# Kernel optimization log

Hardware: AMD Instinct MI355X
Metric: run time of the kernel (lower is better)

The kernel has to match this reference:

```python
import jax, jax.numpy as jnp
import numpy as np

G, N, E = 16, 512, 2048        # graphs, nodes/graph, edges/graph
CN, CE = 64, 64                # node / edge feature channels
K = 3                          # Laguerre polynomial order
RATIO = 0.5
KEEP = int(np.ceil(RATIO * N)) # 256 kept nodes per graph (static)
POWER_ITERS = 64               # power iteration approximating eigsh(k=1,'LM')


def setup_inputs() -> dict:
    key = jax.random.key(0)
    ks = jax.random.split(key, 10)
    x_n = jax.random.normal(ks[0], (G * N, CN), jnp.float32)
    x_e = jax.random.normal(ks[1], (G * E, CE), jnp.float32)
    # incidence endpoints per edge, local node ids, no self loops
    u = jax.random.randint(ks[2], (G, E), 0, N)
    v = (u + 1 + jax.random.randint(ks[3], (G, E), 0, N - 1)) % N
    # node-level conv graph (global ids within per-graph blocks): both directions
    offs = (jnp.arange(G) * N)[:, None]
    src_n = jnp.concatenate([(u + offs).reshape(-1), (v + offs).reshape(-1)])
    dst_n = jnp.concatenate([(v + offs).reshape(-1), (u + offs).reshape(-1)])
    edge_weight_n = jax.random.uniform(ks[4], (src_n.shape[0],), jnp.float32)
    # edge-level conv graph (global ids within per-graph edge blocks)
    ME = 4 * E
    offs_e = (jnp.arange(G) * E)[:, None]
    src_e = (jax.random.randint(ks[5], (G, ME), 0, E) + offs_e).reshape(-1)
    dst_e = (jax.random.randint(ks[6], (G, ME), 0, E) + offs_e).reshape(-1)
    edge_weight_e = jax.random.uniform(ks[7], (src_e.shape[0],), jnp.float32)
    # HodgeLaguerreConv(C -> 1, K) weights (glorot-ish) + bias (zeros init)
    W_n = jax.random.normal(ks[8], (K, CN), jnp.float32) / np.sqrt(CN)
    b_n = jnp.zeros((1,), jnp.float32)
    W_e = jax.random.normal(ks[9], (K, CE), jnp.float32) / np.sqrt(CE)
    b_e = jnp.zeros((1,), jnp.float32)
    return dict(x_n=x_n, x_e=x_e, edge_u=u, edge_v=v,
                src_n=src_n, dst_n=dst_n, edge_weight_n=edge_weight_n,
                src_e=src_e, dst_e=dst_e, edge_weight_e=edge_weight_e,
                W_n=W_n, b_n=b_n, W_e=W_e, b_e=b_e)


def hodge_laguerre(x, src, dst, w, Wk, b):
    """HodgeLaguerreConv with out_channels=1: out = sum_k T_k(L) x @ Wk[k] + b.
    T_0 = x; T_1 = x - Lx; T_{k+1} = (-L T_k + (2k+1) T_k - k T_{k-1})/(k+1)."""
    num = x.shape[0]
    def L(z):  # scatter-add message passing: out[i] = sum_{j->i} norm * z[j]
        return jax.ops.segment_sum(w[:, None] * z[src], dst, num_segments=num)
    Tx0 = x
    out = Tx0 @ Wk[0]
    Tx1 = x - L(x)
    out = out + Tx1 @ Wk[1]
    k = 1
    for i in range(2, Wk.shape[0]):
        Tx2 = (-L(Tx1) + (2 * k + 1) * Tx1 - k * Tx0) / (k + 1)
        out = out + Tx2 @ Wk[i]
        Tx0, Tx1 = Tx1, Tx2
        k += 1
    return out + b[0]


def pool_graph(sn, se, xn, xe, u, v):
    # node score augmented by |B1| @ edge_score (abs incidence gathers both endpoints)
    aug = sn.at[u].add(se).at[v].add(se)
    perm = jnp.argsort(-aug)                    # descending sort, take top KEEP
    mask_n = jnp.zeros((N,), xn.dtype).at[perm[:KEEP]].set(1.0)
    # mask_e = |B1|^T (1 - mask_n); keep edge iff both endpoints kept (== 0)
    bad = (1.0 - mask_n[u]) + (1.0 - mask_n[v])
    keep_e = (bad == 0.0).astype(xn.dtype)
    # dense incidence B1 [N, E]: -1 at source row, +1 at target row
    cols = jnp.arange(E)
    B = jnp.zeros((N, E), xn.dtype).at[u, cols].add(-1.0).at[v, cols].add(1.0)
    Bm = B * mask_n[:, None] * keep_e[None, :]  # row/col masking (zero-padded)
    L0 = Bm @ Bm.T                              # [N, N] node Laplacian
    L1 = Bm.T @ Bm                              # [E, E] edge Laplacian
    # power iteration for lambda_max(L0) (== eigsh k=1 'LM'; zero rows keep spectrum)
    w = jnp.ones((N,), xn.dtype) / np.sqrt(N)
    for _ in range(POWER_ITERS):
        w = L0 @ w
        w = w / (jnp.linalg.norm(w) + 1e-12)
    lam = w @ (L0 @ w)
    scale = 2.0 / (lam + 1e-12)
    return xn * mask_n[:, None], L0 * scale, xe * keep_e[:, None], L1 * scale


def reference(x_n, x_e, edge_u, edge_v, src_n, dst_n, edge_weight_n,
              src_e, dst_e, edge_weight_e, W_n, b_n, W_e, b_e):
    score_n = jax.nn.sigmoid(hodge_laguerre(x_n, src_n, dst_n, edge_weight_n, W_n, b_n).reshape(-1))
    score_e = jax.nn.sigmoid(hodge_laguerre(x_e, src_e, dst_e, edge_weight_e, W_e, b_e).reshape(-1))
    xn_g = (x_n * score_n[:, None]).reshape(G, N, CN)
    xe_g = (x_e * score_e[:, None]).reshape(G, E, CE)
    sn = score_n.reshape(G, N)
    se = score_e.reshape(G, E)
    return jax.vmap(pool_graph)(sn, se, xn_g, xe_g, edge_u, edge_v)
```

## Files before the change

### kernel.cpp

```cpp
#include <hip/hip_runtime.h>
#include <math.h>

#define GG 16
#define NNODE 512
#define EEDGE 2048
#define KEEPN 256
#define PITERS 64
#define NNT 8192
#define NET 32768

#define WS_C1N 0
#define WS_C2N 8192
#define WS_BN  16384
#define WS_C1E 24576
#define WS_C2E 57344
#define WS_BE  90112
#define WS_SNW 122880
#define WS_SEW 131072
#define WS_KLIST 163840
#define WS_KCNT 196608
#define WS_SCALE 196624

#define O_XN 0
#define O_L0 524288
#define O_XE 4718592
#define O_L1 6815744

#define L04 1048576
#define ZTOT4 17825792

__global__ __launch_bounds__(256) void k_dots(const float* __restrict__ xn,
    const float* __restrict__ xe, const float* __restrict__ Wn,
    const float* __restrict__ We, float* __restrict__ ws) {
  int gw = (blockIdx.x * 256 + threadIdx.x) >> 6;
  int lane = threadIdx.x & 63;
  const float* x; const float* W; int row; float *c1, *c2, *bs;
  if (gw < NNT) {
    row = gw; x = xn + (size_t)row * 64; W = Wn;
    c1 = ws + WS_C1N; c2 = ws + WS_C2N; bs = ws + WS_BN;
  } else {
    row = gw - NNT;
    x = xe + (size_t)row * 64; W = We;
    c1 = ws + WS_C1E; c2 = ws + WS_C2E; bs = ws + WS_BE;
  }
  float v = x[lane];
  float r0 = v * W[lane];
  float r1 = v * W[64 + lane];
  float r2 = v * W[128 + lane];
  for (int o = 32; o; o >>= 1) {
    r0 += __shfl_xor(r0, o, 64);
    r1 += __shfl_xor(r1, o, 64);
    r2 += __shfl_xor(r2, o, 64);
  }
  if (lane == 0) { c1[row] = r1; c2[row] = r2; bs[row] = r0 + r1 + r2; }
}

#define SB 3104
__global__ __launch_bounds__(512) void k_pool(
    const int* __restrict__ src_n, const int* __restrict__ dst_n, const float* __restrict__ wn,
    const int* __restrict__ src_e, const int* __restrict__ dst_e, const float* __restrict__ we,
    const int* __restrict__ edge_u, const int* __restrict__ edge_v,
    const float* __restrict__ bnp, const float* __restrict__ bep,
    float* __restrict__ ws, float* __restrict__ out) {
  const int tid = threadIdx.x;
  if (blockIdx.x >= 16) {
    float4 z = make_float4(0.f, 0.f, 0.f, 0.f);
    float4* o4 = (float4*)out;
    int start = (blockIdx.x - 16) * 512 + tid;
    for (int i = start; i < ZTOT4; i += 2048 * 512) {
      int f = (i < L04) ? (O_L0 / 4 + i) : (O_L1 / 4 + (i - L04));
      o4[f] = z;
    }
    return;
  }
  __shared__ float smem[13856];
  int* smi = (int*)smem;
  float* seS = smem;
  float* aug = smem + 2048;
  float* snw = smem + 2560;
  float* red = smem + 3072;
  int*   iws = smi + 3080;
  int*   kcp = smi + 3088;
  float* c1n = smem + SB;        float* c2n = smem + SB + 512;
  float* d1n = smem + SB + 1024; float* d2n = smem + SB + 1536;
  float* e2n = smem + SB + 2048;
  float* c1e = smem + SB;        float* c2e = smem + SB + 2048;
  float* d1e = smem + SB + 4096; float* d2e = smem + SB + 6144;
  float* e2e = smem + SB + 8192;
  int* suL  = smi + SB;          int* svL  = smi + SB + 2048;
  int* maskS = smi + SB + 4096;  int* degS = smi + SB + 4608;
  int* offS = smi + SB + 5120;   int* adj  = smi + SB + 5632;
  float* wvA = smem + SB + 9728; float* wvB = smem + SB + 10240;

  const int g = blockIdx.x;
  const int roffN = g * NNODE;
  const int roffE = g * EEDGE;
  const int lane = tid & 63, wid = tid >> 6;

  if (tid < NNODE) {
    c1n[tid] = ws[WS_C1N + roffN + tid];
    c2n[tid] = ws[WS_C2N + roffN + tid];
    d1n[tid] = 0.f; d2n[tid] = 0.f; e2n[tid] = 0.f;
  }
  __syncthreads();
  for (int t = tid; t < 4096; t += 512) {
    int idx = (t < 2048) ? (g * 2048 + t) : (32768 + g * 2048 + (t - 2048));
    int s = src_n[idx] - roffN, d = dst_n[idx] - roffN;
    float w = wn[idx];
    atomicAdd(&d1n[d], w * c1n[s]);
    atomicAdd(&d2n[d], w * c2n[s]);
  }
  __syncthreads();
  for (int t = tid; t < 4096; t += 512) {
    int idx = (t < 2048) ? (g * 2048 + t) : (32768 + g * 2048 + (t - 2048));
    int s = src_n[idx] - roffN, d = dst_n[idx] - roffN;
    atomicAdd(&e2n[d], wn[idx] * d2n[s]);
  }
  __syncthreads();
  float biasN = bnp[0], biasE = bep[0];
  if (tid < NNODE) {
    float t = ws[WS_BN + roffN + tid] - d1n[tid] - 2.0f * d2n[tid]
            + 0.5f * e2n[tid] + biasN;
    float s = 1.0f / (1.0f + expf(-t));
    snw[tid] = s; aug[tid] = s;
  }
  __syncthreads();

  for (int i = tid; i < EEDGE; i += 512) {
    c1e[i] = ws[WS_C1E + roffE + i];
    c2e[i] = ws[WS_C2E + roffE + i];
    d1e[i] = 0.f; d2e[i] = 0.f; e2e[i] = 0.f;
  }
  __syncthreads();
  for (int t = tid; t < 8192; t += 512) {
    int idx = g * 8192 + t;
    int s = src_e[idx] - roffE, d = dst_e[idx] - roffE;
    float w = we[idx];
    atomicAdd(&d1e[d], w * c1e[s]);
    atomicAdd(&d2e[d], w * c2e[s]);
  }
  __syncthreads();
  for (int t = tid; t < 8192; t += 512) {
    int idx = g * 8192 + t;
    int s = src_e[idx] - roffE, d = dst_e[idx] - roffE;
    atomicAdd(&e2e[d], we[idx] * d2e[s]);
  }
  __syncthreads();
  for (int e = tid; e < EEDGE; e += 512) {
    float t = ws[WS_BE + roffE + e] - d1e[e] - 2.0f * d2e[e]
            + 0.5f * e2e[e] + biasE;
    float s = 1.0f / (1.0f + expf(-t));
    seS[e] = s;
    atomicAdd(&aug[edge_u[roffE + e]], s);
    atomicAdd(&aug[edge_v[roffE + e]], s);
  }
  __syncthreads();

  {
    float a = aug[tid];
    int r = 0;
    #pragma unroll 8
    for (int j = 0; j < NNODE; ++j) {
      float b = aug[j];
      r += (b > a) || (b == a && j < tid);
    }
    maskS[tid] = (r < KEEPN) ? 1 : 0;
    degS[tid] = 0;
  }
  for (int e = tid; e < EEDGE; e += 512) {
    suL[e] = edge_u[roffE + e];
    svL[e] = edge_v[roffE + e];
  }
  if (tid == 0) *kcp = 0;
  __syncthreads();
  ws[WS_SNW + roffN + tid] = snw[tid] * (float)maskS[tid];

  int* wsi = (int*)ws;
  for (int e = tid; e < EEDGE; e += 512) {
    int u = suL[e], v = svL[e];
    int k = maskS[u] & maskS[v];
    ws[WS_SEW + roffE + e] = seS[e] * (float)k;
    if (k) {
      int p = atomicAdd(kcp, 1);
      wsi[WS_KLIST + roffE + p] = e;
      atomicAdd(&degS[u], 1);
      atomicAdd(&degS[v], 1);
    }
  }
  __syncthreads();
  if (tid == 0) wsi[WS_KCNT + g] = *kcp;

  int dv = degS[tid];
  int inc = dv;
  for (int o = 1; o < 64; o <<= 1) {
    int t = __shfl_up(inc, o, 64);
    if (lane >= o) inc += t;
  }
  if (lane == 63) iws[wid] = inc;
  __syncthreads();
  int base = 0;
  for (int k = 0; k < wid; ++k) base += iws[k];
  int myStart = base + inc - dv;
  offS[tid] = myStart;
  __syncthreads();

  for (int e = tid; e < EEDGE; e += 512) {
    int u = suL[e], v = svL[e];
    if (maskS[u] & maskS[v]) {
      int pu = atomicAdd(&offS[u], 1); adj[pu] = v;
      int pv = atomicAdd(&offS[v], 1); adj[pv] = u;
    }
  }
  __syncthreads();
  int myDeg = dv;
  int myEnd = offS[tid];

  wvA[tid] = 0.04419417382415922f;
  __syncthreads();
  float* wcur = wvA; float* wnext = wvB;
  for (int it = 0; it < PITERS; ++it) {
    float acc = (float)myDeg * wcur[tid];
    for (int p = myStart; p < myEnd; ++p) acc -= wcur[adj[p]];
    if ((it & 7) == 7) {
      float sq = acc * acc;
      for (int o = 32; o; o >>= 1) sq += __shfl_xor(sq, o, 64);
      if (lane == 0) red[wid] = sq;
      __syncthreads();
      float tot = red[0] + red[1] + red[2] + red[3]
                + red[4] + red[5] + red[6] + red[7];
      wnext[tid] = acc * (1.0f / (sqrtf(tot) + 1e-12f));
    } else {
      wnext[tid] = acc;
    }
    __syncthreads();
    float* tmp = wcur; wcur = wnext; wnext = tmp;
  }
  {
    float wv_ = wcur[tid];
    float acc = (float)myDeg * wv_;
    for (int p = myStart; p < myEnd; ++p) acc -= wcur[adj[p]];
    float pr = wv_ * acc;
    for (int o = 32; o; o >>= 1) pr += __shfl_xor(pr, o, 64);
    if (lane == 0) red[wid] = pr;
    __syncthreads();
    if (tid == 0) {
      float lam = red[0] + red[1] + red[2] + red[3]
                + red[4] + red[5] + red[6] + red[7];
      ws[WS_SCALE + g] = 2.0f / (lam + 1e-12f);
    }
  }
}

__global__ __launch_bounds__(256) void k_out(
    const float* __restrict__ xn, const float* __restrict__ xe,
    const int* __restrict__ edge_u, const int* __restrict__ edge_v,
    const float* __restrict__ ws, float* __restrict__ out) {
  int b = blockIdx.x, tid = threadIdx.x;
  const int* wsi = (const int*)ws;
  if (b < 512) {
    int idx = b * 256 + tid;
    int row = idx >> 4;
    float s = ws[WS_SNW + row];
    float4 x4 = ((const float4*)xn)[idx];
    ((float4*)(out + O_XN))[idx] = make_float4(x4.x * s, x4.y * s, x4.z * s, x4.w * s);
  } else if (b < 2560) {
    int idx = (b - 512) * 256 + tid;
    int row = idx >> 4;
    float s = ws[WS_SEW + row];
    float4 x4 = ((const float4*)xe)[idx];
    ((float4*)(out + O_XE))[idx] = make_float4(x4.x * s, x4.y * s, x4.z * s, x4.w * s);
  } else if (b < 2576) {
    int g = b - 2560;
    int cnt = wsi[WS_KCNT + g];
    float s = ws[WS_SCALE + g];
    float* L0 = out + O_L0 + (long long)g * (NNODE * NNODE);
    const int* kl = wsi + WS_KLIST + g * EEDGE;
    const int* eu = edge_u + g * EEDGE;
    const int* ev = edge_v + g * EEDGE;
    for (int t = tid; t < cnt; t += 256) {
      int e = kl[t];
      int u = eu[e], v = ev[e];
      atomicAdd(&L0[u * NNODE + u], s);
      atomicAdd(&L0[v * NNODE + v], s);
      atomicAdd(&L0[u * NNODE + v], -s);
      atomicAdd(&L0[v * NNODE + u], -s);
    }
  } else {
    int q = b - 2576;
    int g = q >> 8, sb = q & 255;
    int cnt = wsi[WS_KCNT + g];
    float s = ws[WS_SCALE + g];
    float* L1 = out + O_L1 + (long long)g * (EEDGE * EEDGE);
    const int* kl = wsi + WS_KLIST + g * EEDGE;
    const int* eu = edge_u + g * EEDGE;
    const int* ev = edge_v + g * EEDGE;
    for (int a = sb; a < cnt; a += 256) {
      int e1 = kl[a];
      int u1 = eu[e1], v1 = ev[e1];
      long long rowoff = (long long)e1 * EEDGE;
      for (int b2 = tid; b2 < cnt; b2 += 256) {
        int e2 = kl[b2];
        int u2 = eu[e2], v2 = ev[e2];
        int val = (u1 == u2) + (v1 == v2) - (v1 == u2) - (u1 == v2);
        if (val) L1[rowoff + e2] = s * (float)val;
      }
    }
  }
}

extern "C" void kernel_launch(void* const* d_in, const int* in_sizes, int n_in,
                              void* d_out, int out_size, void* d_ws, size_t ws_size,
                              hipStream_t stream) {
  const float* x_n = (const float*)d_in[0];
  const float* x_e = (const float*)d_in[1];
  const int* edge_u = (const int*)d_in[2];
  const int* edge_v = (const int*)d_in[3];
  const int* src_n = (const int*)d_in[4];
  const int* dst_n = (const int*)d_in[5];
  const float* ew_n = (const float*)d_in[6];
  const int* src_e = (const int*)d_in[7];
  const int* dst_e = (const int*)d_in[8];
  const float* ew_e = (const float*)d_in[9];
  const float* W_n = (const float*)d_in[10];
  const float* b_n = (const float*)d_in[11];
  const float* W_e = (const float*)d_in[12];
  const float* b_e = (const float*)d_in[13];
  float* ws = (float*)d_ws;
  float* out = (float*)d_out;

  k_dots<<<10240, 256, 0, stream>>>(x_n, x_e, W_n, W_e, ws);
  k_pool<<<16 + 2048, 512, 0, stream>>>(src_n, dst_n, ew_n, src_e, dst_e, ew_e,
                                        edge_u, edge_v, b_n, b_e, ws, out);
  k_out<<<6672, 256, 0, stream>>>(x_n, x_e, edge_u, edge_v, ws, out);
}
```

Before: 481.7 us.

## Split output zero-fill across kernels, shrink pool shared memory, register-cache neighbor lists

```diff
diff --git a/kernel.cpp b/kernel.cpp
--- a/kernel.cpp
+++ b/kernel.cpp
@@ -8,6 +8,8 @@
 #define PITERS 64
 #define NNT 8192
 #define NET 32768
+
+typedef float vfloat4 __attribute__((ext_vector_type(4)));
 
 #define WS_C1N 0
 #define WS_C2N 8192
@@ -28,10 +30,23 @@
 
 #define L04 1048576
 #define ZTOT4 17825792
+#define ZA4 6291456
 
 __global__ __launch_bounds__(256) void k_dots(const float* __restrict__ xn,
     const float* __restrict__ xe, const float* __restrict__ Wn,
-    const float* __restrict__ We, float* __restrict__ ws) {
+    const float* __restrict__ We, float* __restrict__ ws, float* __restrict__ out) {
+  if (blockIdx.x >= 10240) {
+    vfloat4 z = (vfloat4)(0.f);
+    vfloat4* o4 = (vfloat4*)out;
+    int start = (blockIdx.x - 10240) * 256 + threadIdx.x;
+    #pragma unroll
+    for (int n = 0; n < 24; ++n) {
+      int i = start + n * 262144;
+      int f = (i < L04) ? (O_L0 / 4 + i) : (O_L1 / 4 + (i - L04));
+      __builtin_nontemporal_store(z, &o4[f]);
+    }
+    return;
+  }
   int gw = (blockIdx.x * 256 + threadIdx.x) >> 6;
   int lane = threadIdx.x & 63;
   const float* x; const float* W; int row; float *c1, *c2, *bs;
@@ -55,7 +70,14 @@
   if (lane == 0) { c1[row] = r1; c2[row] = r2; bs[row] = r0 + r1 + r2; }
 }
 
-#define SB 3104
+#define SM_AUG 0
+#define SM_SNW 512
+#define SM_RED 1024
+#define SM_IWS 1032
+#define SM_KCP 1040
+#define SM_S0  1056
+#define SM_TOT 9256
+#define DCAP 12
 __global__ __launch_bounds__(512) void k_pool(
     const int* __restrict__ src_n, const int* __restrict__ dst_n, const float* __restrict__ wn,
     const int* __restrict__ src_e, const int* __restrict__ dst_e, const float* __restrict__ we,
@@ -64,97 +86,110 @@
     float* __restrict__ ws, float* __restrict__ out) {
   const int tid = threadIdx.x;
   if (blockIdx.x >= 16) {
-    float4 z = make_float4(0.f, 0.f, 0.f, 0.f);
-    float4* o4 = (float4*)out;
-    int start = (blockIdx.x - 16) * 512 + tid;
-    for (int i = start; i < ZTOT4; i += 2048 * 512) {
-      int f = (i < L04) ? (O_L0 / 4 + i) : (O_L1 / 4 + (i - L04));
-      o4[f] = z;
+    vfloat4 z = (vfloat4)(0.f);
+    vfloat4* o4 = (vfloat4*)out;
+    int start = ZA4 + (blockIdx.x - 16) * 512 + tid;
+    #pragma unroll
+    for (int n = 0; n < 11; ++n) {
+      int i = start + n * 1048576;
+      __builtin_nontemporal_store(z, &o4[O_L1 / 4 + (i - L04)]);
     }
     return;
   }
-  __shared__ float smem[13856];
+  __shared__ float smem[SM_TOT];
   int* smi = (int*)smem;
-  float* seS = smem;
-  float* aug = smem + 2048;
-  float* snw = smem + 2560;
-  float* red = smem + 3072;
-  int*   iws = smi + 3080;
-  int*   kcp = smi + 3088;
-  float* c1n = smem + SB;        float* c2n = smem + SB + 512;
-  float* d1n = smem + SB + 1024; float* d2n = smem + SB + 1536;
-  float* e2n = smem + SB + 2048;
-  float* c1e = smem + SB;        float* c2e = smem + SB + 2048;
-  float* d1e = smem + SB + 4096; float* d2e = smem + SB + 6144;
-  float* e2e = smem + SB + 8192;
-  int* suL  = smi + SB;          int* svL  = smi + SB + 2048;
-  int* maskS = smi + SB + 4096;  int* degS = smi + SB + 4608;
-  int* offS = smi + SB + 5120;   int* adj  = smi + SB + 5632;
-  float* wvA = smem + SB + 9728; float* wvB = smem + SB + 10240;
+  float* aug = smem + SM_AUG;
+  float* snw = smem + SM_SNW;
+  float* red = smem + SM_RED;
+  int*   iws = smi + SM_IWS;
+  int*   kcp = smi + SM_KCP;
 
   const int g = blockIdx.x;
   const int roffN = g * NNODE;
   const int roffE = g * EEDGE;
   const int lane = tid & 63, wid = tid >> 6;
-
-  if (tid < NNODE) {
+  float biasN = bnp[0], biasE = bep[0];
+
+  {
+    float* c1n = smem + SM_S0;
+    float* c2n = smem + SM_S0 + 512;
+    float* d1n = smem + SM_S0 + 1024;
+    float* d2n = smem + SM_S0 + 1536;
+    float* e2n = smem + SM_S0 + 2048;
     c1n[tid] = ws[WS_C1N + roffN + tid];
     c2n[tid] = ws[WS_C2N + roffN + tid];
     d1n[tid] = 0.f; d2n[tid] = 0.f; e2n[tid] = 0.f;
-  }
-  __syncthreads();
-  for (int t = tid; t < 4096; t += 512) {
-    int idx = (t < 2048) ? (g * 2048 + t) : (32768 + g * 2048 + (t - 2048));
-    int s = src_n[idx] - roffN, d = dst_n[idx] - roffN;
-    float w = wn[idx];
-    atomicAdd(&d1n[d], w * c1n[s]);
-    atomicAdd(&d2n[d], w * c2n[s]);
-  }
-  __syncthreads();
-  for (int t = tid; t < 4096; t += 512) {
-    int idx = (t < 2048) ? (g * 2048 + t) : (32768 + g * 2048 + (t - 2048));
-    int s = src_n[idx] - roffN, d = dst_n[idx] - roffN;
-    atomicAdd(&e2n[d], wn[idx] * d2n[s]);
-  }
-  __syncthreads();
-  float biasN = bnp[0], biasE = bep[0];
-  if (tid < NNODE) {
+    __syncthreads();
+    for (int t = tid; t < 4096; t += 512) {
+      int idx = (t < 2048) ? (g * 2048 + t) : (32768 + g * 2048 + (t - 2048));
+      int s = src_n[idx] - roffN, d = dst_n[idx] - roffN;
+      float w = wn[idx];
+      atomicAdd(&d1n[d], w * c1n[s]);
+      atomicAdd(&d2n[d], w * c2n[s]);
+    }
+    __syncthreads();
+    for (int t = tid; t < 4096; t += 512) {
+      int idx = (t < 2048) ? (g * 2048 + t) : (32768 + g * 2048 + (t - 2048));
+      int s = src_n[idx] - roffN, d = dst_n[idx] - roffN;
+      atomicAdd(&e2n[d], wn[idx] * d2n[s]);
+    }
+    __syncthreads();
     float t = ws[WS_BN + roffN + tid] - d1n[tid] - 2.0f * d2n[tid]
             + 0.5f * e2n[tid] + biasN;
     float s = 1.0f / (1.0f + expf(-t));
     snw[tid] = s; aug[tid] = s;
-  }
-  __syncthreads();
-
-  for (int i = tid; i < EEDGE; i += 512) {
-    c1e[i] = ws[WS_C1E + roffE + i];
-    c2e[i] = ws[WS_C2E + roffE + i];
-    d1e[i] = 0.f; d2e[i] = 0.f; e2e[i] = 0.f;
-  }
-  __syncthreads();
-  for (int t = tid; t < 8192; t += 512) {
-    int idx = g * 8192 + t;
-    int s = src_e[idx] - roffE, d = dst_e[idx] - roffE;
-    float w = we[idx];
-    atomicAdd(&d1e[d], w * c1e[s]);
-    atomicAdd(&d2e[d], w * c2e[s]);
-  }
-  __syncthreads();
-  for (int t = tid; t < 8192; t += 512) {
-    int idx = g * 8192 + t;
-    int s = src_e[idx] - roffE, d = dst_e[idx] - roffE;
-    atomicAdd(&e2e[d], we[idx] * d2e[s]);
-  }
-  __syncthreads();
-  for (int e = tid; e < EEDGE; e += 512) {
-    float t = ws[WS_BE + roffE + e] - d1e[e] - 2.0f * d2e[e]
-            + 0.5f * e2e[e] + biasE;
-    float s = 1.0f / (1.0f + expf(-t));
-    seS[e] = s;
-    atomicAdd(&aug[edge_u[roffE + e]], s);
-    atomicAdd(&aug[edge_v[roffE + e]], s);
-  }
-  __syncthreads();
+    __syncthreads();
+  }
+
+  float* seS = smem + SM_S0 + 2048;
+  int*   suv = smi + SM_S0;
+  {
+    float* c1e = smem + SM_S0;
+    float* c2e = smem + SM_S0 + 2048;
+    float* d1e = smem + SM_S0 + 4096;
+    float* d2e = smem + SM_S0 + 6144;
+    float* e2e = smem + SM_S0;
+    for (int i = tid; i < EEDGE; i += 512) {
+      c1e[i] = ws[WS_C1E + roffE + i];
+      c2e[i] = ws[WS_C2E + roffE + i];
+      d1e[i] = 0.f; d2e[i] = 0.f;
+    }
+    __syncthreads();
+    for (int t = tid; t < 8192; t += 512) {
+      int idx = g * 8192 + t;
+      int s = src_e[idx] - roffE, d = dst_e[idx] - roffE;
+      float w = we[idx];
+      atomicAdd(&d1e[d], w * c1e[s]);
+      atomicAdd(&d2e[d], w * c2e[s]);
+    }
+    __syncthreads();
+    for (int i = tid; i < EEDGE; i += 512) e2e[i] = 0.f;
+    __syncthreads();
+    for (int t = tid; t < 8192; t += 512) {
+      int idx = g * 8192 + t;
+      int s = src_e[idx] - roffE, d = dst_e[idx] - roffE;
+      atomicAdd(&e2e[d], we[idx] * d2e[s]);
+    }
+    __syncthreads();
+    for (int e = tid; e < EEDGE; e += 512) {
+      float t = ws[WS_BE + roffE + e] - d1e[e] - 2.0f * d2e[e]
+              + 0.5f * e2e[e] + biasE;
+      float s = 1.0f / (1.0f + expf(-t));
+      int u = edge_u[roffE + e], v = edge_v[roffE + e];
+      seS[e] = s;
+      suv[e] = u | (v << 16);
+      atomicAdd(&aug[u], s);
+      atomicAdd(&aug[v], s);
+    }
+    __syncthreads();
+  }
+
+  unsigned short* adjU = (unsigned short*)(smem + SM_S0 + 4096);
+  float* wvA = smem + SM_S0 + 6144;
+  float* wvB = smem + SM_S0 + 6660;
+  int* maskS = smi + SM_S0 + 7176;
+  int* degS  = smi + SM_S0 + 7688;
+  int* offS  = smi + SM_SNW;
 
   {
     float a = aug[tid];
@@ -167,17 +202,14 @@
     maskS[tid] = (r < KEEPN) ? 1 : 0;
     degS[tid] = 0;
   }
-  for (int e = tid; e < EEDGE; e += 512) {
-    suL[e] = edge_u[roffE + e];
-    svL[e] = edge_v[roffE + e];
-  }
   if (tid == 0) *kcp = 0;
   __syncthreads();
   ws[WS_SNW + roffN + tid] = snw[tid] * (float)maskS[tid];
 
   int* wsi = (int*)ws;
   for (int e = tid; e < EEDGE; e += 512) {
-    int u = suL[e], v = svL[e];
+    int p2 = suv[e];
+    int u = p2 & 0xffff, v = p2 >> 16;
     int k = maskS[u] & maskS[v];
     ws[WS_SEW + roffE + e] = seS[e] * (float)k;
     if (k) {
@@ -205,22 +237,32 @@
   __syncthreads();
 
   for (int e = tid; e < EEDGE; e += 512) {
-    int u = suL[e], v = svL[e];
+    int p2 = suv[e];
+    int u = p2 & 0xffff, v = p2 >> 16;
     if (maskS[u] & maskS[v]) {
-      int pu = atomicAdd(&offS[u], 1); adj[pu] = v;
-      int pv = atomicAdd(&offS[v], 1); adj[pv] = u;
+      int pu = atomicAdd(&offS[u], 1); adjU[pu] = (unsigned short)v;
+      int pv = atomicAdd(&offS[v], 1); adjU[pv] = (unsigned short)u;
     }
   }
   __syncthreads();
   int myDeg = dv;
-  int myEnd = offS[tid];
+  int myEnd = myStart + myDeg;
+
+  int nbr[DCAP];
+  #pragma unroll
+  for (int k = 0; k < DCAP; ++k)
+    nbr[k] = (k < myDeg) ? (int)adjU[myStart + k] : NNODE;
+  bool ovf = myDeg > DCAP;
 
   wvA[tid] = 0.04419417382415922f;
+  if (tid == 0) { wvA[NNODE] = 0.f; wvB[NNODE] = 0.f; }
   __syncthreads();
   float* wcur = wvA; float* wnext = wvB;
   for (int it = 0; it < PITERS; ++it) {
     float acc = (float)myDeg * wcur[tid];
-    for (int p = myStart; p < myEnd; ++p) acc -= wcur[adj[p]];
+    #pragma unroll
+    for (int k = 0; k < DCAP; ++k) acc -= wcur[nbr[k]];
+    if (ovf) for (int p = myStart + DCAP; p < myEnd; ++p) acc -= wcur[(int)adjU[p]];
     if ((it & 7) == 7) {
       float sq = acc * acc;
       for (int o = 32; o; o >>= 1) sq += __shfl_xor(sq, o, 64);
@@ -238,7 +280,9 @@
   {
     float wv_ = wcur[tid];
     float acc = (float)myDeg * wv_;
-    for (int p = myStart; p < myEnd; ++p) acc -= wcur[adj[p]];
+    #pragma unroll
+    for (int k = 0; k < DCAP; ++k) acc -= wcur[nbr[k]];
+    if (ovf) for (int p = myStart + DCAP; p < myEnd; ++p) acc -= wcur[(int)adjU[p]];
     float pr = wv_ * acc;
     for (int o = 32; o; o >>= 1) pr += __shfl_xor(pr, o, 64);
     if (lane == 0) red[wid] = pr;
@@ -328,7 +372,7 @@
   float* ws = (float*)d_ws;
   float* out = (float*)d_out;
 
-  k_dots<<<10240, 256, 0, stream>>>(x_n, x_e, W_n, W_e, ws);
+  k_dots<<<10240 + 1024, 256, 0, stream>>>(x_n, x_e, W_n, W_e, ws, out);
   k_pool<<<16 + 2048, 512, 0, stream>>>(src_n, dst_n, ew_n, src_e, dst_e, ew_e,
                                         edge_u, edge_v, b_n, b_e, ws, out);
   k_out<<<6672, 256, 0, stream>>>(x_n, x_e, edge_u, edge_v, ws, out);
```

After: 470.4 us. 2.3% less time.
